# Performance work log

Measured on AMD Instinct MI355X. Metric: run time of the kernel, lower is better.

## Reference

```python
import jax, jax.numpy as jnp
import numpy as np

B, D, H, NSTEPS = 4096, 512, 2048, 16


def setup_inputs() -> dict:
    key = jax.random.key(0)
    k1, k2, k3, k4 = jax.random.split(key, 4)
    s_x = 1.0 / np.sqrt(D)
    s_h = 1.0 / np.sqrt(H)
    return {
        "z_in": jax.random.normal(k1, (B, D), dtype=jnp.float32),
        "Wx": jax.random.normal(k2, (D, H), dtype=jnp.float32) * s_x,
        "Wh": jax.random.normal(k3, (H, H), dtype=jnp.float32) * s_h,
        "bh": jnp.zeros((H,), dtype=jnp.float32),
        "Wout": jax.random.normal(k4, (H, D), dtype=jnp.float32) * s_h,
        "bout": jnp.zeros((D,), dtype=jnp.float32),
        "n_steps": NSTEPS,
    }


def reference(z_in, Wx, Wh, bh, Wout, bout, n_steps):
    # Input projection is identical every step (same z_in fed each iteration).
    xproj = z_in @ Wx + bh  # [B, H]
    h0 = jnp.zeros((z_in.shape[0], Wh.shape[0]), dtype=z_in.dtype)

    def step(h, _):
        h_new = jnp.tanh(xproj + h @ Wh)          # Elman RNN cell, hidden retained
        out = h_new @ Wout + bout                  # MLP head hidden -> latent
        return h_new, out

    _, outs = jax.lax.scan(step, h0, None, length=n_steps)  # [n_steps, B, D]
    return jnp.transpose(outs, (1, 0, 2))  # torch.stack(outs, 1) -> [B, n_steps, D]
```

## Files before the change

kernel.cpp:

```cpp
#include <hip/hip_runtime.h>
#include <hip/hip_bf16.h>
#include <stdint.h>

#define B_ 4096
#define D_ 512
#define H_ 2048
#define NS_ 16

typedef __bf16 bf16x8 __attribute__((ext_vector_type(8)));
typedef float f32x4 __attribute__((ext_vector_type(4)));
typedef short short4v __attribute__((ext_vector_type(4)));

__device__ __forceinline__ short f2bf(float f) {
  union { float f; uint32_t u; } c; c.f = f;
  uint32_t u = c.u;
  return (short)((u + 0x7fffu + ((u >> 16) & 1u)) >> 16);
}

__device__ __forceinline__ float tanh_fast(float x) {
  float e = __expf(2.0f * x);
  return 1.0f - 2.0f / (e + 1.0f);
}

__device__ __forceinline__ void gload16(const void* g, void* l) {
  __builtin_amdgcn_global_load_lds((const __attribute__((address_space(1))) void*)g,
                                   (__attribute__((address_space(3))) void*)l,
                                   16, 0, 0);
}

__global__ __launch_bounds__(512, 2) void gemm256_fused(
    const short* __restrict__ A, const short* __restrict__ Bt, int K,
    const float* __restrict__ xproj, const float* __restrict__ bias,
    float* __restrict__ outf, short* __restrict__ outh, int tout, int gridN)
{
  __shared__ short lds[65536];
  char* const lbase = (char*)lds;
  const int tid = threadIdx.x, lane = tid & 63, wid = tid >> 6;
  const int wm = wid >> 2, wn = wid & 3;

  const int nwg = gridDim.x;
  const int cpx = nwg >> 3;
  const int swz = ((int)blockIdx.x & 7) * cpx + ((int)blockIdx.x >> 3);
  const int tm = swz / gridN, tn = swz % gridN;
  const int row0 = tm * 256, col0 = tn * 256;

  const int NT = K >> 5;

  const int rA0 = wid * 32 + (lane >> 2);
  const int rA1 = rA0 + 16;
  const int sl = lane & 3;
  const short* gA0 = A  + (size_t)(row0 + rA0) * K + ((sl ^ ((rA0 >> 1) & 3)) << 3);
  const short* gA1 = A  + (size_t)(row0 + rA1) * K + ((sl ^ ((rA1 >> 1) & 3)) << 3);
  const short* gB0 = Bt + (size_t)(col0 + rA0) * K + ((sl ^ ((rA0 >> 1) & 3)) << 3);
  const short* gB1 = Bt + (size_t)(col0 + rA1) * K + ((sl ^ ((rA1 >> 1) & 3)) << 3);

  const int rr = lane & 15, s = lane >> 4;
  int offA[8], offB[4];
#pragma unroll
  for (int m = 0; m < 8; ++m) {
    int r = wm * 128 + m * 16 + rr;
    offA[m] = r * 64 + ((s ^ ((r >> 1) & 3)) << 4);
  }
#pragma unroll
  for (int n = 0; n < 4; ++n) {
    int r = wn * 64 + n * 16 + rr;
    offB[n] = 16384 + r * 64 + ((s ^ ((r >> 1) & 3)) << 4);
  }

  f32x4 acc[8][4];
#pragma unroll
  for (int m = 0; m < 8; ++m)
#pragma unroll
    for (int n = 0; n < 4; ++n)
      acc[m][n] = (f32x4){0.f, 0.f, 0.f, 0.f};

  auto stageA = [&](int kt) {
    char* da = lbase + (kt & 3) * 32768 + wid * 2048;
    gload16(gA0 + (size_t)kt * 32, da);
    gload16(gA1 + (size_t)kt * 32, da + 1024);
  };
  auto stageB = [&](int kt) {
    char* db = lbase + (kt & 3) * 32768 + 16384 + wid * 2048;
    gload16(gB0 + (size_t)kt * 32, db);
    gload16(gB1 + (size_t)kt * 32, db + 1024);
  };

  stageA(0); stageB(0);
  stageA(1); stageB(1);
  stageA(2); stageB(2);

  auto tile = [&](int kt, bool issue) {
    __builtin_amdgcn_sched_barrier(0);
    __builtin_amdgcn_s_barrier();
    __builtin_amdgcn_sched_barrier(0);
    const char* lb = lbase + (kt & 3) * 32768;
    if (issue) stageA(kt + 3);
    bf16x8 a[4], b[4];
#pragma unroll
    for (int m = 0; m < 4; ++m) a[m] = *(const bf16x8*)(lb + offA[m]);
#pragma unroll
    for (int n = 0; n < 4; ++n) b[n] = *(const bf16x8*)(lb + offB[n]);
    __builtin_amdgcn_s_setprio(1);
#pragma unroll
    for (int m = 0; m < 4; ++m)
#pragma unroll
      for (int n = 0; n < 4; ++n)
        acc[m][n] = __builtin_amdgcn_mfma_f32_16x16x32_bf16(a[m], b[n], acc[m][n], 0, 0, 0);
    __builtin_amdgcn_s_setprio(0);
    __builtin_amdgcn_sched_barrier(0);
    if (issue) stageB(kt + 3);
#pragma unroll
    for (int m = 0; m < 4; ++m) a[m] = *(const bf16x8*)(lb + offA[4 + m]);
    __builtin_amdgcn_s_setprio(1);
#pragma unroll
    for (int m = 0; m < 4; ++m)
#pragma unroll
      for (int n = 0; n < 4; ++n)
        acc[4 + m][n] = __builtin_amdgcn_mfma_f32_16x16x32_bf16(a[m], b[n], acc[4 + m][n], 0, 0, 0);
    __builtin_amdgcn_s_setprio(0);
    __builtin_amdgcn_sched_barrier(0);
  };

  int kt = 0;
  for (; kt < NT - 3; ++kt) {
    asm volatile("s_waitcnt vmcnt(8)" ::: "memory");
    tile(kt, true);
  }
  asm volatile("s_waitcnt vmcnt(8)" ::: "memory");
  tile(NT - 3, false);
  asm volatile("s_waitcnt vmcnt(4)" ::: "memory");
  tile(NT - 2, false);
  asm volatile("s_waitcnt vmcnt(0)" ::: "memory");
  tile(NT - 1, false);

  const int rb = row0 + wm * 128 + ((lane >> 4) << 2);
  const int cb = col0 + wn * 64 + (lane & 15);
#pragma unroll
  for (int m = 0; m < 8; ++m) {
#pragma unroll
    for (int n = 0; n < 4; ++n) {
      const int col = cb + n * 16;
#pragma unroll
      for (int r = 0; r < 4; ++r) {
        const int row = rb + m * 16 + r;
        float v = acc[m][n][r];
        if (col < H_) {
          float x = xproj[(size_t)row * H_ + col];
          outh[(size_t)row * H_ + col] = f2bf(tanh_fast(x + v));
        } else {
          int oc = col - H_;
          outf[(size_t)row * (NS_ * D_) + tout * D_ + oc] = v + bias[oc];
        }
      }
    }
  }
}

template<int BM, int BN, int EPI>
__global__ __launch_bounds__(256, 2) void gemm_bt(
    const short* __restrict__ A, const short* __restrict__ Bt, int K,
    const float* __restrict__ xproj, const float* __restrict__ bias,
    float* __restrict__ outf, short* __restrict__ outh, int ldN, int tout)
{
  constexpr int WM = BM / 2, WN = BN / 2;
  constexpr int RM = WM / 16, RN = WN / 16;
  __shared__ short lds[2][(BM + BN) * 32];
  const int tid = threadIdx.x, lane = tid & 63, wid = tid >> 6;
  const int wm = wid >> 1, wn = wid & 1;
  const int row0 = blockIdx.y * BM, col0 = blockIdx.x * BN;
  const short* Ag = A + (size_t)row0 * K;
  const short* Bg = Bt + (size_t)col0 * K;

  f32x4 acc[RM][RN];
#pragma unroll
  for (int m = 0; m < RM; ++m)
#pragma unroll
    for (int n = 0; n < RN; ++n)
      acc[m][n] = (f32x4){0.f, 0.f, 0.f, 0.f};

  const int nt = K >> 5;

  auto stage = [&](int kt, int buf) {
    const short* ga = Ag + (kt << 5);
#pragma unroll
    for (int i = 0; i < BM * 4; i += 256) {
      int slot = i + tid;
      gload16(ga + (size_t)(slot >> 2) * K + ((slot & 3) << 3), &lds[buf][slot * 8]);
    }
    const short* gb = Bg + (kt << 5);
#pragma unroll
    for (int i = 0; i < BN * 4; i += 256) {
      int slot = i + tid;
      gload16(gb + (size_t)(slot >> 2) * K + ((slot & 3) << 3),
              &lds[buf][BM * 32 + slot * 8]);
    }
  };

  stage(0, 0);
  __syncthreads();
  int cur = 0;
  const int kq = (lane >> 4) << 3;
  const int rr = lane & 15;
  for (int kt = 0; kt < nt; ++kt) {
    if (kt + 1 < nt) stage(kt + 1, cur ^ 1);
    const short* la = &lds[cur][(wm * WM) * 32];
    const short* lb = &lds[cur][BM * 32 + (wn * WN) * 32];
    bf16x8 a[RM], b[RN];
#pragma unroll
    for (int m = 0; m < RM; ++m)
      a[m] = *(const bf16x8*)(la + (m * 16 + rr) * 32 + kq);
#pragma unroll
    for (int n = 0; n < RN; ++n)
      b[n] = *(const bf16x8*)(lb + (n * 16 + rr) * 32 + kq);
#pragma unroll
    for (int m = 0; m < RM; ++m)
#pragma unroll
      for (int n = 0; n < RN; ++n)
        acc[m][n] = __builtin_amdgcn_mfma_f32_16x16x32_bf16(a[m], b[n], acc[m][n], 0, 0, 0);
    __syncthreads();
    cur ^= 1;
  }

  const int rb = row0 + wm * WM + ((lane >> 4) << 2);
  const int cb = col0 + wn * WN + (lane & 15);
#pragma unroll
  for (int m = 0; m < RM; ++m) {
#pragma unroll
    for (int n = 0; n < RN; ++n) {
      const int col = cb + n * 16;
#pragma unroll
      for (int r = 0; r < 4; ++r) {
        const int row = rb + m * 16 + r;
        float v = acc[m][n][r];
        if (EPI == 0) {
          outf[(size_t)row * ldN + col] = v + bias[col];
        } else {
          outf[(size_t)row * (NS_ * D_) + tout * D_ + col] = v + bias[col];
        }
      }
    }
  }
}

__global__ void transpose_cvt(const float* __restrict__ in, short* __restrict__ out,
                              int R, int C) {
  __shared__ float tile[32][33];
  const int tx = threadIdx.x & 31, ty = threadIdx.x >> 5;
  const int c0 = blockIdx.x * 32, r0 = blockIdx.y * 32;
#pragma unroll
  for (int i = 0; i < 32; i += 8)
    tile[ty + i][tx] = in[(size_t)(r0 + ty + i) * C + c0 + tx];
  __syncthreads();
#pragma unroll
  for (int i = 0; i < 32; i += 8)
    out[(size_t)(c0 + ty + i) * R + r0 + tx] = f2bf(tile[tx][ty + i]);
}

__global__ void cvt_bf16_k(const float4* __restrict__ in, short4v* __restrict__ out, int n4) {
  int i = blockIdx.x * 256 + threadIdx.x;
  if (i >= n4) return;
  float4 v = in[i];
  short4v o;
  o[0] = f2bf(v.x); o[1] = f2bf(v.y); o[2] = f2bf(v.z); o[3] = f2bf(v.w);
  out[i] = o;
}

__global__ void tanh_h0_k(const float4* __restrict__ xp, short4v* __restrict__ h, int n4) {
  int i = blockIdx.x * 256 + threadIdx.x;
  if (i >= n4) return;
  float4 v = xp[i];
  short4v o;
  o[0] = f2bf(tanh_fast(v.x)); o[1] = f2bf(tanh_fast(v.y));
  o[2] = f2bf(tanh_fast(v.z)); o[3] = f2bf(tanh_fast(v.w));
  h[i] = o;
}

extern "C" void kernel_launch(void* const* d_in, const int* in_sizes, int n_in,
                              void* d_out, int out_size, void* d_ws, size_t ws_size,
                              hipStream_t stream) {
  const float* z    = (const float*)d_in[0];
  const float* Wx   = (const float*)d_in[1];
  const float* Wh   = (const float*)d_in[2];
  const float* bh   = (const float*)d_in[3];
  const float* Wout = (const float*)d_in[4];
  const float* bout = (const float*)d_in[5];
  float* out = (float*)d_out;

  short* zb    = (short*)d_ws;
  short* WxT   = zb + (size_t)B_ * D_;
  short* WcatT = WxT + (size_t)H_ * D_;
  short* WoutT = WcatT + (size_t)H_ * H_;
  short* h0    = WcatT + (size_t)(H_ + D_) * H_;
  short* h1    = h0 + (size_t)B_ * H_;
  float* xproj = (float*)(h1 + (size_t)B_ * H_);

  cvt_bf16_k<<<(B_ * D_ / 4 + 255) / 256, 256, 0, stream>>>((const float4*)z, (short4v*)zb, B_ * D_ / 4);
  transpose_cvt<<<dim3(H_ / 32, D_ / 32), 256, 0, stream>>>(Wx, WxT, D_, H_);
  transpose_cvt<<<dim3(H_ / 32, H_ / 32), 256, 0, stream>>>(Wh, WcatT, H_, H_);
  transpose_cvt<<<dim3(D_ / 32, H_ / 32), 256, 0, stream>>>(Wout, WoutT, H_, D_);

  gemm_bt<128, 128, 0><<<dim3(H_ / 128, B_ / 128), 256, 0, stream>>>(
      zb, WxT, D_, nullptr, bh, xproj, nullptr, H_, 0);
  tanh_h0_k<<<(B_ * H_ / 4 + 255) / 256, 256, 0, stream>>>((const float4*)xproj, (short4v*)h0, B_ * H_ / 4);

  short* hb[2] = {h0, h1};
  for (int t = 1; t <= 15; ++t) {
    const short* hp = hb[(t - 1) & 1];
    short* hn = hb[t & 1];
    gemm256_fused<<<160, 512, 0, stream>>>(
        hp, WcatT, H_, xproj, bout, out, hn, t - 1, 10);
  }
  gemm_bt<128, 64, 2><<<dim3(D_ / 64, B_ / 128), 256, 0, stream>>>(
      hb[1], WoutT, H_, nullptr, bout, out, nullptr, 0, 15);
}
```

Before: 1.424 ms.

## Restructure GEMM main loop into ping-pong phases with explicit LDS address space

Replaces the tile lambda with one loop that splits each K-tile into two phases, each fenced by workgroup barriers. LDS fragment reads are issued before the barrier and awaited with lgkmcnt(0), and the global-to-LDS prefetch waits are folded into the loop. LDS accesses now go through short indices with an address_space(3) pointer type, so the compiler can emit ds_read directly instead of generic flat loads. The intent is to overlap LDS reads with barrier waits and synchronize waves in a ping-pong style for better MFMA issue, at the cost of extra barriers per iteration.

New measurement: 1.524 ms. 7.0% more time.

```diff
diff --git a/kernel.cpp b/kernel.cpp
--- a/kernel.cpp
+++ b/kernel.cpp
@@ -10,6 +10,7 @@
 typedef __bf16 bf16x8 __attribute__((ext_vector_type(8)));
 typedef float f32x4 __attribute__((ext_vector_type(4)));
 typedef short short4v __attribute__((ext_vector_type(4)));
+typedef __attribute__((address_space(3))) const bf16x8* lds_frag_p;
 
 __device__ __forceinline__ short f2bf(float f) {
   union { float f; uint32_t u; } c; c.f = f;
@@ -34,7 +35,6 @@
     float* __restrict__ outf, short* __restrict__ outh, int tout, int gridN)
 {
   __shared__ short lds[65536];
-  char* const lbase = (char*)lds;
   const int tid = threadIdx.x, lane = tid & 63, wid = tid >> 6;
   const int wm = wid >> 2, wn = wid & 3;
 
@@ -54,17 +54,17 @@
   const short* gB0 = Bt + (size_t)(col0 + rA0) * K + ((sl ^ ((rA0 >> 1) & 3)) << 3);
   const short* gB1 = Bt + (size_t)(col0 + rA1) * K + ((sl ^ ((rA1 >> 1) & 3)) << 3);
 
-  const int rr = lane & 15, s = lane >> 4;
+  const int rr = lane & 15, s4 = lane >> 4;
   int offA[8], offB[4];
 #pragma unroll
   for (int m = 0; m < 8; ++m) {
     int r = wm * 128 + m * 16 + rr;
-    offA[m] = r * 64 + ((s ^ ((r >> 1) & 3)) << 4);
+    offA[m] = r * 32 + ((s4 ^ ((r >> 1) & 3)) << 3);
   }
 #pragma unroll
   for (int n = 0; n < 4; ++n) {
     int r = wn * 64 + n * 16 + rr;
-    offB[n] = 16384 + r * 64 + ((s ^ ((r >> 1) & 3)) << 4);
+    offB[n] = 8192 + r * 32 + ((s4 ^ ((r >> 1) & 3)) << 3);
   }
 
   f32x4 acc[8][4];
@@ -75,31 +75,35 @@
       acc[m][n] = (f32x4){0.f, 0.f, 0.f, 0.f};
 
   auto stageA = [&](int kt) {
-    char* da = lbase + (kt & 3) * 32768 + wid * 2048;
-    gload16(gA0 + (size_t)kt * 32, da);
-    gload16(gA1 + (size_t)kt * 32, da + 1024);
+    int d = (kt & 3) * 16384 + wid * 1024;
+    gload16(gA0 + (size_t)kt * 32, &lds[d]);
+    gload16(gA1 + (size_t)kt * 32, &lds[d + 512]);
   };
   auto stageB = [&](int kt) {
-    char* db = lbase + (kt & 3) * 32768 + 16384 + wid * 2048;
-    gload16(gB0 + (size_t)kt * 32, db);
-    gload16(gB1 + (size_t)kt * 32, db + 1024);
+    int d = (kt & 3) * 16384 + 8192 + wid * 1024;
+    gload16(gB0 + (size_t)kt * 32, &lds[d]);
+    gload16(gB1 + (size_t)kt * 32, &lds[d + 512]);
   };
 
   stageA(0); stageB(0);
   stageA(1); stageB(1);
   stageA(2); stageB(2);
-
-  auto tile = [&](int kt, bool issue) {
+  asm volatile("s_waitcnt vmcnt(8)" ::: "memory");
+  __builtin_amdgcn_s_barrier();
+
+  bf16x8 a[4], b[4];
+  for (int kt = 0; kt < NT; ++kt) {
+    const int bb = (kt & 3) * 16384;
+    const bool st = (kt < NT - 3);
+#pragma unroll
+    for (int m = 0; m < 4; ++m) a[m] = *(lds_frag_p)&lds[bb + offA[m]];
+#pragma unroll
+    for (int n = 0; n < 4; ++n) b[n] = *(lds_frag_p)&lds[bb + offB[n]];
+    if (st) stageA(kt + 3);
     __builtin_amdgcn_sched_barrier(0);
     __builtin_amdgcn_s_barrier();
+    asm volatile("s_waitcnt lgkmcnt(0)" ::: "memory");
     __builtin_amdgcn_sched_barrier(0);
-    const char* lb = lbase + (kt & 3) * 32768;
-    if (issue) stageA(kt + 3);
-    bf16x8 a[4], b[4];
-#pragma unroll
-    for (int m = 0; m < 4; ++m) a[m] = *(const bf16x8*)(lb + offA[m]);
-#pragma unroll
-    for (int n = 0; n < 4; ++n) b[n] = *(const bf16x8*)(lb + offB[n]);
     __builtin_amdgcn_s_setprio(1);
 #pragma unroll
     for (int m = 0; m < 4; ++m)
@@ -107,10 +111,21 @@
       for (int n = 0; n < 4; ++n)
         acc[m][n] = __builtin_amdgcn_mfma_f32_16x16x32_bf16(a[m], b[n], acc[m][n], 0, 0, 0);
     __builtin_amdgcn_s_setprio(0);
+    __builtin_amdgcn_s_barrier();
+#pragma unroll
+    for (int m = 0; m < 4; ++m) a[m] = *(lds_frag_p)&lds[bb + offA[4 + m]];
+    if (st) {
+      stageB(kt + 3);
+      asm volatile("s_waitcnt vmcnt(8)" ::: "memory");
+    } else if (kt == NT - 3) {
+      asm volatile("s_waitcnt vmcnt(4)" ::: "memory");
+    } else if (kt == NT - 2) {
+      asm volatile("s_waitcnt vmcnt(0)" ::: "memory");
+    }
     __builtin_amdgcn_sched_barrier(0);
-    if (issue) stageB(kt + 3);
-#pragma unroll
-    for (int m = 0; m < 4; ++m) a[m] = *(const bf16x8*)(lb + offA[4 + m]);
+    __builtin_amdgcn_s_barrier();
+    asm volatile("s_waitcnt lgkmcnt(0)" ::: "memory");
+    __builtin_amdgcn_sched_barrier(0);
     __builtin_amdgcn_s_setprio(1);
 #pragma unroll
     for (int m = 0; m < 4; ++m)
@@ -118,20 +133,8 @@
       for (int n = 0; n < 4; ++n)
         acc[4 + m][n] = __builtin_amdgcn_mfma_f32_16x16x32_bf16(a[m], b[n], acc[4 + m][n], 0, 0, 0);
     __builtin_amdgcn_s_setprio(0);
-    __builtin_amdgcn_sched_barrier(0);
-  };
-
-  int kt = 0;
-  for (; kt < NT - 3; ++kt) {
-    asm volatile("s_waitcnt vmcnt(8)" ::: "memory");
-    tile(kt, true);
-  }
-  asm volatile("s_waitcnt vmcnt(8)" ::: "memory");
-  tile(NT - 3, false);
-  asm volatile("s_waitcnt vmcnt(4)" ::: "memory");
-  tile(NT - 2, false);
-  asm volatile("s_waitcnt vmcnt(0)" ::: "memory");
-  tile(NT - 1, false);
+    __builtin_amdgcn_s_barrier();
+  }
 
   const int rb = row0 + wm * 128 + ((lane >> 4) << 2);
   const int cb = col0 + wn * 64 + (lane & 15);
```
